# Optimization experiments

Measured on AMD Instinct MI355X. Metric: run time of the kernel, lower is better.

The kernel has to match this reference:

```python
import jax, jax.numpy as jnp
import numpy as np

B, N, C, S = 16, 1024, 16, 8
TYPE_DIM, TOK_DIM, D, O = 128, 128, 256, 256
NUM_TYPES, NUM_TOKENS, L = 200, 50000, 2
NEG = -1000000000000.0


def setup_inputs() -> dict:
    key = jax.random.key(0)
    ks = jax.random.split(key, 8)
    node_type = jax.random.randint(ks[0], (B, N), 0, NUM_TYPES)
    node_tokens = jax.random.randint(ks[1], (B, N, S), 0, NUM_TOKENS)
    children_index = jax.random.randint(ks[2], (B, N, C), 0, N)
    # padding_idx=0 -> row 0 of both embedding tables is zero
    type_table = (0.02 * jax.random.normal(ks[3], (NUM_TYPES, TYPE_DIM))).at[0].set(0.0)
    token_table = (0.02 * jax.random.normal(ks[4], (NUM_TOKENS, TOK_DIM))).at[0].set(0.0)
    W_parent = 0.02 * jax.random.normal(ks[5], (TYPE_DIM + TOK_DIM, D))
    b_parent = jnp.zeros((D,), jnp.float32)
    conv_w = 0.02 * jax.random.normal(ks[6], (L, 3, D, O))  # stacked [w_t, w_r, w_l] per layer
    conv_b = jnp.zeros((L, O), jnp.float32)
    attn_a = 0.02 * jax.random.normal(ks[7], (O,))
    return dict(node_type=node_type, node_tokens=node_tokens, children_index=children_index,
                type_table=type_table, token_table=token_table, W_parent=W_parent,
                b_parent=b_parent, conv_w=conv_w, conv_b=conv_b, attn_a=attn_a)


def _gather_children(parent, idx):
    # parent: [B,N,Dim]; idx: [B,N,C] with 0 meaning 'no child' (zero vector)
    lookup = parent.at[:, 0, :].set(0.0)
    return jax.vmap(lambda v, i: v[i])(lookup, idx)  # [B,N,C,Dim]


def _tbcnn_coef(children):
    # Standard TBCNN positional coefficients over [parent, child_1..child_C].
    b, n, c = children.shape
    f = jnp.float32
    cmask = (children > 0).astype(f)                                      # [B,N,C]
    mask = jnp.concatenate([jnp.zeros((b, n, 1), f), cmask], axis=2)      # [B,N,C+1]
    eta_t = jnp.concatenate([jnp.ones((b, n, 1), f), jnp.zeros((b, n, c), f)], axis=2)
    num_sib = jnp.sum(cmask, axis=2, keepdims=True)                       # [B,N,1]
    pos = jnp.arange(-1.0, c, dtype=f)                                    # [-1,0,...,C-1]
    child_idx = pos[None, None, :] * mask
    singles = jnp.concatenate([jnp.zeros((b, n, 1), f), jnp.full((b, n, 1), 0.5, f),
                               jnp.zeros((b, n, c - 1), f)], axis=2)
    denom = jnp.maximum(num_sib - 1.0, 1.0)
    eta_r = jnp.where(num_sib == 1.0, singles, mask * child_idx / denom)
    eta_l = (1.0 - eta_t) * (1.0 - eta_r) * mask
    return jnp.stack([eta_t, eta_r, eta_l], axis=3)                       # [B,N,C+1,3]


def _forward(node_type, node_tokens, children_index, type_table, token_table,
             W_parent, b_parent, conv_w, conv_b, attn_a):
    # --- embeddings + parent projection ---
    type_emb = type_table[node_type]                       # [B,N,TYPE_DIM]
    tok_emb = token_table[node_tokens].sum(axis=2)         # [B,N,TOK_DIM] (sum over subtokens)
    parent = jnp.concatenate([type_emb, tok_emb], axis=-1) @ W_parent + b_parent  # [B,N,D]
    # --- tree convolutions ---
    coef = _tbcnn_coef(children_index)                     # [B,N,C+1,3]
    nodes = parent
    ch = _gather_children(nodes, children_index)           # [B,N,C,D]
    n_layers = conv_w.shape[0]
    for l in range(n_layers):
        tree = jnp.concatenate([nodes[:, :, None, :], ch], axis=2)  # [B,N,C+1,D]
        mixed = jnp.einsum('bnck,bncd->bnkd', coef, tree)           # [B,N,3,D]
        nodes = jnp.tanh(jnp.einsum('bnkd,kdo->bno', mixed, conv_w[l]) + conv_b[l])
        if l < n_layers - 1:
            ch = _gather_children(nodes, children_index)
    # --- attention aggregation ---
    m = (node_type != 0)[..., None]                        # [B,N,1] bool
    score = jnp.einsum('bno,o->bn', nodes, attn_a)[..., None]
    score = jnp.where(m, score, NEG)
    w = jax.nn.sigmoid(score)
    code_vector = jnp.mean(nodes * m * w, axis=1)          # [B,O]
    return code_vector, nodes


def reference(node_type, node_tokens, children_index, type_table, token_table,
              W_parent, b_parent, conv_w, conv_b, attn_a):
    return _forward(node_type, node_tokens, children_index, type_table, token_table,
                    W_parent, b_parent, conv_w, conv_b, attn_a)
```

## Files before the change

### kernel.cpp

```cpp
#include <hip/hip_runtime.h>
#include <hip/hip_fp16.h>
#include <math.h>

constexpr int Bsz = 16, Nn = 1024, Cc = 16, Ss = 8;
constexpr int BN = Bsz * Nn;
constexpr int EQ = 32;
constexpr int CQ = 32;

typedef __attribute__((ext_vector_type(8))) short bf16x8;
typedef __attribute__((ext_vector_type(4))) float f32x4;
typedef __attribute__((ext_vector_type(4))) unsigned short u16x4;

__device__ inline unsigned short f2bf_rne(float x) {
    unsigned u = __builtin_bit_cast(unsigned, x);
    unsigned r = (u + 0x7FFFu + ((u >> 16) & 1u)) >> 16;
    return (unsigned short)r;
}
__device__ inline float bf2f(unsigned short h) {
    unsigned u = ((unsigned)h) << 16;
    return __builtin_bit_cast(float, u);
}

__global__ __launch_bounds__(256) void pack_all_kernel(
    const float* __restrict__ conv_w,
    const float* __restrict__ Wp,
    unsigned short* __restrict__ whi, unsigned short* __restrict__ wpq)
{
    if (blockIdx.x < 192) {
        const int t = blockIdx.x * 256 + threadIdx.x;
        const int col = t & 255;
        const int gg  = (t >> 8) & 3;
        const int kb  = (t >> 10) % 24;
        const int l   = t / (24 * 4 * 256);
        const float* W = conv_w + (size_t)l * 768 * 256;
        const size_t dst = (size_t)t * 8;
        #pragma unroll
        for (int i = 0; i < 8; ++i)
            whi[dst + i] = f2bf_rne(W[(size_t)(kb * 32 + gg * 8 + i) * 256 + col]);
    } else {
        const int t = (blockIdx.x - 192) * 256 + threadIdx.x;
        const int col = t & 255;
        const int gg  = (t >> 8) & 3;
        const int kb  = t >> 10;
        const size_t dst = (size_t)t * 8;
        #pragma unroll
        for (int i = 0; i < 8; ++i)
            wpq[dst + i] = f2bf_rne(Wp[(size_t)(kb * 32 + gg * 8 + i) * 256 + col]);
    }
}

__global__ __launch_bounds__(256, 4) void emb_mfma_kernel(
    const int* __restrict__ node_type, const int* __restrict__ node_tokens,
    const float* __restrict__ type_table, const float* __restrict__ token_table,
    const unsigned short* __restrict__ wpq,
    const float* __restrict__ bp,
    unsigned short* __restrict__ outh)
{
    constexpr int AP = 264;
    __shared__ unsigned short A[EQ][AP];

    const int tid  = threadIdx.x;
    const int lane = tid & 63;
    const int w    = tid >> 6;
    const int g0   = blockIdx.x * EQ;

    #pragma unroll
    for (int it = 0; it < 8; ++it) {
        const int r = w * 8 + it;
        const int gnode = g0 + r;
        if (lane < 32) {
            const int tt = node_type[gnode];
            const float4 v = *reinterpret_cast<const float4*>(
                type_table + (size_t)tt * 128 + lane * 4);
            u16x4 s;
            s.x = f2bf_rne(v.x); s.y = f2bf_rne(v.y);
            s.z = f2bf_rne(v.z); s.w = f2bf_rne(v.w);
            *reinterpret_cast<u16x4*>(&A[r][lane * 4]) = s;
        } else {
            const int q = lane - 32;
            float4 acc = {0.f, 0.f, 0.f, 0.f};
            #pragma unroll
            for (int si = 0; si < Ss; ++si) {
                const int tok = node_tokens[gnode * Ss + si];
                const float4 v = *reinterpret_cast<const float4*>(
                    token_table + (size_t)tok * 128 + q * 4);
                acc.x += v.x; acc.y += v.y; acc.z += v.z; acc.w += v.w;
            }
            u16x4 s;
            s.x = f2bf_rne(acc.x); s.y = f2bf_rne(acc.y);
            s.z = f2bf_rne(acc.z); s.w = f2bf_rne(acc.w);
            *reinterpret_cast<u16x4*>(&A[r][128 + q * 4]) = s;
        }
    }
    __syncthreads();

    const int colg = w * 64;
    const int rr   = lane & 15;
    const int g    = lane >> 4;

    const unsigned short* pwh = wpq + ((size_t)(g * 256 + colg + rr)) * 8;

    f32x4 acc[2][4];
    #pragma unroll
    for (int t = 0; t < 2; ++t)
        #pragma unroll
        for (int f = 0; f < 4; ++f) acc[t][f] = (f32x4){0.f, 0.f, 0.f, 0.f};

    bf16x8 bA[4], bB[4];
    #pragma unroll
    for (int f = 0; f < 4; ++f)
        bA[f] = *reinterpret_cast<const bf16x8*>(pwh + f * 128);

    for (int kb = 0; kb < 8; kb += 2) {
        {
            const int o1 = (kb + 1) * 8192;
            #pragma unroll
            for (int f = 0; f < 4; ++f)
                bB[f] = *reinterpret_cast<const bf16x8*>(pwh + o1 + f * 128);
        }
        {
            const int k0 = kb * 32 + g * 8;
            const bf16x8 a0 = *reinterpret_cast<const bf16x8*>(&A[rr][k0]);
            const bf16x8 a1 = *reinterpret_cast<const bf16x8*>(&A[16 + rr][k0]);
            #pragma unroll
            for (int f = 0; f < 4; ++f) {
                acc[0][f] = __builtin_amdgcn_mfma_f32_16x16x32_bf16(a0, bA[f], acc[0][f], 0, 0, 0);
                acc[1][f] = __builtin_amdgcn_mfma_f32_16x16x32_bf16(a1, bA[f], acc[1][f], 0, 0, 0);
            }
        }
        if (kb + 2 < 8) {
            const int o2 = (kb + 2) * 8192;
            #pragma unroll
            for (int f = 0; f < 4; ++f)
                bA[f] = *reinterpret_cast<const bf16x8*>(pwh + o2 + f * 128);
        }
        {
            const int k0 = (kb + 1) * 32 + g * 8;
            const bf16x8 a0 = *reinterpret_cast<const bf16x8*>(&A[rr][k0]);
            const bf16x8 a1 = *reinterpret_cast<const bf16x8*>(&A[16 + rr][k0]);
            #pragma unroll
            for (int f = 0; f < 4; ++f) {
                acc[0][f] = __builtin_amdgcn_mfma_f32_16x16x32_bf16(a0, bB[f], acc[0][f], 0, 0, 0);
                acc[1][f] = __builtin_amdgcn_mfma_f32_16x16x32_bf16(a1, bB[f], acc[1][f], 0, 0, 0);
            }
        }
    }

    #pragma unroll
    for (int t = 0; t < 2; ++t)
        #pragma unroll
        for (int f = 0; f < 4; ++f) {
            const int col = colg + f * 16 + rr;
            const float bv = bp[col];
            #pragma unroll
            for (int i = 0; i < 4; ++i) {
                const int row = t * 16 + g * 4 + i;
                outh[(size_t)(g0 + row) * 256 + col] = f2bf_rne(acc[t][f][i] + bv);
            }
        }
}

template<int FUSE>
__global__ __launch_bounds__(512, 4) void conv_mfma_kernel(
    const unsigned short* __restrict__ in_h,
    const int* __restrict__ children_index,
    const unsigned short* __restrict__ whi,
    const float* __restrict__ bias,
    unsigned short* __restrict__ out_h,
    float* __restrict__ out_f,
    const int* __restrict__ node_type,
    const float* __restrict__ attn_a,
    float* __restrict__ partial)
{
    constexpr int AP = 776;
    __shared__ unsigned short Ahi[CQ][AP];
    __shared__ unsigned short idx_s[CQ][Cc];
    __shared__ __half eta_s[2][CQ][Cc];
    __shared__ float sc_lds[8][CQ];
    __shared__ float wm_lds[CQ];

    const int tid = threadIdx.x;

    const int P = blockIdx.x;
    const int xx = P & 7;
    const int rst = P >> 3;
    const int j = rst & 31;
    const int yy = rst >> 5;
    const int batch = xx + 8 * yy;
    const int g0 = batch * Nn + j * CQ;
    const unsigned short* inb = in_h + (size_t)batch * Nn * 256;

    {
        const int r = tid >> 4, c = tid & 15;
        idx_s[r][c] = (unsigned short)children_index[(size_t)(g0 + r) * Cc + c];
    }
    __syncthreads();
    {
        const int r = tid >> 4, c = tid & 15;
        int ns = 0;
        #pragma unroll
        for (int q = 0; q < Cc; ++q) ns += (idx_s[r][q] > 0) ? 1 : 0;
        const bool cm = idx_s[r][c] > 0;
        float er;
        if (ns == 1) {
            er = (c == 0) ? 0.5f : 0.f;
        } else {
            const float denom = (float)((ns - 1 > 1) ? (ns - 1) : 1);
            er = (float)c / denom;
        }
        eta_s[0][r][c] = __float2half(cm ? er : 0.f);
        eta_s[1][r][c] = __float2half(cm ? (1.f - er) : 0.f);
    }
    __syncthreads();

    {
        const int q = tid & 63;
        const int rgrp = tid >> 6;
        #pragma unroll
        for (int rr4 = 0; rr4 < 4; ++rr4) {
            const int r = rgrp * 4 + rr4;
            const u16x4 m0h = *reinterpret_cast<const u16x4*>(
                in_h + (size_t)(g0 + r) * 256 + q * 4);
            float4 m1 = {0.f, 0.f, 0.f, 0.f};
            float4 m2 = {0.f, 0.f, 0.f, 0.f};
            #pragma unroll
            for (int c = 0; c < Cc; ++c) {
                const int ci = idx_s[r][c];
                const u16x4 vh = *reinterpret_cast<const u16x4*>(
                    inb + (size_t)ci * 256 + q * 4);
                const float vx = bf2f(vh.x), vy = bf2f(vh.y);
                const float vz = bf2f(vh.z), vw = bf2f(vh.w);
                const float er = __half2float(eta_s[0][r][c]);
                const float el = __half2float(eta_s[1][r][c]);
                m1.x = fmaf(er, vx, m1.x); m1.y = fmaf(er, vy, m1.y);
                m1.z = fmaf(er, vz, m1.z); m1.w = fmaf(er, vw, m1.w);
                m2.x = fmaf(el, vx, m2.x); m2.y = fmaf(el, vy, m2.y);
                m2.z = fmaf(el, vz, m2.z); m2.w = fmaf(el, vw, m2.w);
            }
            u16x4 s1, s2;
            s1.x = f2bf_rne(m1.x); s1.y = f2bf_rne(m1.y);
            s1.z = f2bf_rne(m1.z); s1.w = f2bf_rne(m1.w);
            s2.x = f2bf_rne(m2.x); s2.y = f2bf_rne(m2.y);
            s2.z = f2bf_rne(m2.z); s2.w = f2bf_rne(m2.w);
            *reinterpret_cast<u16x4*>(&Ahi[r][q * 4])       = m0h;
            *reinterpret_cast<u16x4*>(&Ahi[r][256 + q * 4]) = s1;
            *reinterpret_cast<u16x4*>(&Ahi[r][512 + q * 4]) = s2;
        }
    }
    __syncthreads();

    const int lane = tid & 63;
    const int w    = tid >> 6;
    const int colg = w * 32;
    const int rr   = lane & 15;
    const int g    = lane >> 4;

    const unsigned short* pwh = whi + ((size_t)(g * 256 + colg + rr)) * 8;

    f32x4 acc[2][2];
    #pragma unroll
    for (int t = 0; t < 2; ++t)
        #pragma unroll
        for (int f = 0; f < 2; ++f) acc[t][f] = (f32x4){0.f, 0.f, 0.f, 0.f};

    bf16x8 bA[2], bB[2];
    #pragma unroll
    for (int f = 0; f < 2; ++f)
        bA[f] = *reinterpret_cast<const bf16x8*>(pwh + f * 128);

    for (int kb = 0; kb < 24; kb += 2) {
        {
            const int o1 = (kb + 1) * 8192;
            #pragma unroll
            for (int f = 0; f < 2; ++f)
                bB[f] = *reinterpret_cast<const bf16x8*>(pwh + o1 + f * 128);
        }
        {
            const int k0 = kb * 32 + g * 8;
            const bf16x8 a0 = *reinterpret_cast<const bf16x8*>(&Ahi[rr][k0]);
            const bf16x8 a1 = *reinterpret_cast<const bf16x8*>(&Ahi[16 + rr][k0]);
            #pragma unroll
            for (int f = 0; f < 2; ++f) {
                acc[0][f] = __builtin_amdgcn_mfma_f32_16x16x32_bf16(a0, bA[f], acc[0][f], 0, 0, 0);
                acc[1][f] = __builtin_amdgcn_mfma_f32_16x16x32_bf16(a1, bA[f], acc[1][f], 0, 0, 0);
            }
        }
        if (kb + 2 < 24) {
            const int o2 = (kb + 2) * 8192;
            #pragma unroll
            for (int f = 0; f < 2; ++f)
                bA[f] = *reinterpret_cast<const bf16x8*>(pwh + o2 + f * 128);
        }
        {
            const int k0 = (kb + 1) * 32 + g * 8;
            const bf16x8 a0 = *reinterpret_cast<const bf16x8*>(&Ahi[rr][k0]);
            const bf16x8 a1 = *reinterpret_cast<const bf16x8*>(&Ahi[16 + rr][k0]);
            #pragma unroll
            for (int f = 0; f < 2; ++f) {
                acc[0][f] = __builtin_amdgcn_mfma_f32_16x16x32_bf16(a0, bB[f], acc[0][f], 0, 0, 0);
                acc[1][f] = __builtin_amdgcn_mfma_f32_16x16x32_bf16(a1, bB[f], acc[1][f], 0, 0, 0);
            }
        }
    }

    float nd[2][2][4];
    #pragma unroll
    for (int t = 0; t < 2; ++t)
        #pragma unroll
        for (int f = 0; f < 2; ++f) {
            const int col = colg + f * 16 + rr;
            const float bv = bias[col];
            #pragma unroll
            for (int i = 0; i < 4; ++i) {
                const int row = t * 16 + g * 4 + i;
                const float v = tanhf(acc[t][f][i] + bv);
                nd[t][f][i] = v;
                if (FUSE) out_f[(size_t)(g0 + row) * 256 + col] = v;
                else      out_h[(size_t)(g0 + row) * 256 + col] = f2bf_rne(v);
            }
        }

    if (FUSE) {
        float av[2];
        #pragma unroll
        for (int f = 0; f < 2; ++f) av[f] = attn_a[colg + f * 16 + rr];

        float s[2][4];
        #pragma unroll
        for (int t = 0; t < 2; ++t)
            #pragma unroll
            for (int i = 0; i < 4; ++i) {
                float v = 0.f;
                #pragma unroll
                for (int f = 0; f < 2; ++f) v = fmaf(nd[t][f][i], av[f], v);
                s[t][i] = v;
            }
        #pragma unroll
        for (int off = 1; off < 16; off <<= 1)
            #pragma unroll
            for (int t = 0; t < 2; ++t)
                #pragma unroll
                for (int i = 0; i < 4; ++i)
                    s[t][i] += __shfl_xor(s[t][i], off, 64);
        if (rr == 0) {
            #pragma unroll
            for (int t = 0; t < 2; ++t)
                #pragma unroll
                for (int i = 0; i < 4; ++i)
                    sc_lds[w][t * 16 + g * 4 + i] = s[t][i];
        }
        __syncthreads();
        if (tid < CQ) {
            float sc = 0.f;
            #pragma unroll
            for (int ww = 0; ww < 8; ++ww) sc += sc_lds[ww][tid];
            float wmv = 0.f;
            if (node_type[g0 + tid] != 0) wmv = 1.f / (1.f + expf(-sc));
            wm_lds[tid] = wmv;
        }
        __syncthreads();

        float qf[2];
        #pragma unroll
        for (int f = 0; f < 2; ++f) {
            float v = 0.f;
            #pragma unroll
            for (int t = 0; t < 2; ++t)
                #pragma unroll
                for (int i = 0; i < 4; ++i)
                    v = fmaf(wm_lds[t * 16 + g * 4 + i], nd[t][f][i], v);
            qf[f] = v;
        }
        #pragma unroll
        for (int f = 0; f < 2; ++f) {
            qf[f] += __shfl_xor(qf[f], 16, 64);
            qf[f] += __shfl_xor(qf[f], 32, 64);
        }
        if (g == 0) {
            const int pidx = batch * 32 + j;
            #pragma unroll
            for (int f = 0; f < 2; ++f)
                partial[(size_t)pidx * 256 + colg + f * 16 + rr] = qf[f];
        }
    }
}

__global__ __launch_bounds__(256) void final_kernel(
    const float* __restrict__ partial, float* __restrict__ code)
{
    const int i = blockIdx.x * 256 + threadIdx.x;
    const int b = i >> 8, o = i & 255;
    float acc = 0.f;
    #pragma unroll
    for (int c = 0; c < 32; ++c) acc += partial[(size_t)(b * 32 + c) * 256 + o];
    code[i] = acc * (1.f / 1024.f);
}

extern "C" void kernel_launch(void* const* d_in, const int* in_sizes, int n_in,
                              void* d_out, int out_size, void* d_ws, size_t ws_size,
                              hipStream_t stream)
{
    const int*   node_type   = (const int*)d_in[0];
    const int*   node_tokens = (const int*)d_in[1];
    const int*   children    = (const int*)d_in[2];
    const float* type_table  = (const float*)d_in[3];
    const float* token_table = (const float*)d_in[4];
    const float* Wp          = (const float*)d_in[5];
    const float* bp          = (const float*)d_in[6];
    const float* conv_w      = (const float*)d_in[7];
    const float* conv_b      = (const float*)d_in[8];
    const float* attn_a      = (const float*)d_in[9];

    float* out    = (float*)d_out;
    float* code   = out;
    float* nodesF = out + 4096;

    unsigned short* nodes0 = (unsigned short*)d_ws;
    unsigned short* nodes1 = nodes0 + (size_t)BN * 256;
    float* partial = (float*)(nodes1 + (size_t)BN * 256);
    unsigned short* whi = (unsigned short*)(partial + 512 * 256);
    unsigned short* wpq = whi + 2 * 196608;

    constexpr int LSTRIDE = 196608;

    pack_all_kernel<<<224, 256, 0, stream>>>(conv_w, Wp, whi, wpq);

    emb_mfma_kernel<<<BN / EQ, 256, 0, stream>>>(
        node_type, node_tokens, type_table, token_table, wpq, bp, nodes0);

    conv_mfma_kernel<0><<<BN / CQ, 512, 0, stream>>>(
        nodes0, children, whi, conv_b, nodes1,
        nullptr, nullptr, nullptr, nullptr);

    conv_mfma_kernel<1><<<BN / CQ, 512, 0, stream>>>(
        nodes1, children, whi + LSTRIDE, conv_b + 256, nullptr,
        nodesF, node_type, attn_a, partial);

    final_kernel<<<16, 256, 0, stream>>>(partial, code);
}
```

Baseline: 77.58 us.

## Halve embedding tile rows, use fast tanh/sigmoid, fp32 eta, MFMA priority

```diff
diff --git a/kernel.cpp b/kernel.cpp
--- a/kernel.cpp
+++ b/kernel.cpp
@@ -1,10 +1,9 @@
 #include <hip/hip_runtime.h>
-#include <hip/hip_fp16.h>
 #include <math.h>
 
 constexpr int Bsz = 16, Nn = 1024, Cc = 16, Ss = 8;
 constexpr int BN = Bsz * Nn;
-constexpr int EQ = 32;
+constexpr int EQ = 16;
 constexpr int CQ = 32;
 
 typedef __attribute__((ext_vector_type(8))) short bf16x8;
@@ -19,6 +18,12 @@
 __device__ inline float bf2f(unsigned short h) {
     unsigned u = ((unsigned)h) << 16;
     return __builtin_bit_cast(float, u);
+}
+__device__ inline float fast_tanh(float x) {
+    const float ax = fabsf(x);
+    const float t  = __expf(-2.f * ax);
+    const float r  = __fdividef(1.f - t, 1.f + t);
+    return copysignf(r, x);
 }
 
 __global__ __launch_bounds__(256) void pack_all_kernel(
@@ -65,8 +70,8 @@
     const int g0   = blockIdx.x * EQ;
 
     #pragma unroll
-    for (int it = 0; it < 8; ++it) {
-        const int r = w * 8 + it;
+    for (int it = 0; it < 4; ++it) {
+        const int r = w * 4 + it;
         const int gnode = g0 + r;
         if (lane < 32) {
             const int tt = node_type[gnode];
@@ -100,11 +105,9 @@
 
     const unsigned short* pwh = wpq + ((size_t)(g * 256 + colg + rr)) * 8;
 
-    f32x4 acc[2][4];
-    #pragma unroll
-    for (int t = 0; t < 2; ++t)
-        #pragma unroll
-        for (int f = 0; f < 4; ++f) acc[t][f] = (f32x4){0.f, 0.f, 0.f, 0.f};
+    f32x4 acc[4];
+    #pragma unroll
+    for (int f = 0; f < 4; ++f) acc[f] = (f32x4){0.f, 0.f, 0.f, 0.f};
 
     bf16x8 bA[4], bB[4];
     #pragma unroll
@@ -120,13 +123,10 @@
         }
         {
             const int k0 = kb * 32 + g * 8;
-            const bf16x8 a0 = *reinterpret_cast<const bf16x8*>(&A[rr][k0]);
-            const bf16x8 a1 = *reinterpret_cast<const bf16x8*>(&A[16 + rr][k0]);
-            #pragma unroll
-            for (int f = 0; f < 4; ++f) {
-                acc[0][f] = __builtin_amdgcn_mfma_f32_16x16x32_bf16(a0, bA[f], acc[0][f], 0, 0, 0);
-                acc[1][f] = __builtin_amdgcn_mfma_f32_16x16x32_bf16(a1, bA[f], acc[1][f], 0, 0, 0);
-            }
+            const bf16x8 ah = *reinterpret_cast<const bf16x8*>(&A[rr][k0]);
+            #pragma unroll
+            for (int f = 0; f < 4; ++f)
+                acc[f] = __builtin_amdgcn_mfma_f32_16x16x32_bf16(ah, bA[f], acc[f], 0, 0, 0);
         }
         if (kb + 2 < 8) {
             const int o2 = (kb + 2) * 8192;
@@ -136,28 +136,23 @@
         }
         {
             const int k0 = (kb + 1) * 32 + g * 8;
-            const bf16x8 a0 = *reinterpret_cast<const bf16x8*>(&A[rr][k0]);
-            const bf16x8 a1 = *reinterpret_cast<const bf16x8*>(&A[16 + rr][k0]);
-            #pragma unroll
-            for (int f = 0; f < 4; ++f) {
-                acc[0][f] = __builtin_amdgcn_mfma_f32_16x16x32_bf16(a0, bB[f], acc[0][f], 0, 0, 0);
-                acc[1][f] = __builtin_amdgcn_mfma_f32_16x16x32_bf16(a1, bB[f], acc[1][f], 0, 0, 0);
-            }
-        }
-    }
-
-    #pragma unroll
-    for (int t = 0; t < 2; ++t)
-        #pragma unroll
-        for (int f = 0; f < 4; ++f) {
-            const int col = colg + f * 16 + rr;
-            const float bv = bp[col];
-            #pragma unroll
-            for (int i = 0; i < 4; ++i) {
-                const int row = t * 16 + g * 4 + i;
-                outh[(size_t)(g0 + row) * 256 + col] = f2bf_rne(acc[t][f][i] + bv);
-            }
-        }
+            const bf16x8 ah = *reinterpret_cast<const bf16x8*>(&A[rr][k0]);
+            #pragma unroll
+            for (int f = 0; f < 4; ++f)
+                acc[f] = __builtin_amdgcn_mfma_f32_16x16x32_bf16(ah, bB[f], acc[f], 0, 0, 0);
+        }
+    }
+
+    #pragma unroll
+    for (int f = 0; f < 4; ++f) {
+        const int col = colg + f * 16 + rr;
+        const float bv = bp[col];
+        #pragma unroll
+        for (int i = 0; i < 4; ++i) {
+            const int row = g * 4 + i;
+            outh[(size_t)(g0 + row) * 256 + col] = f2bf_rne(acc[f][i] + bv);
+        }
+    }
 }
 
 template<int FUSE>
@@ -175,7 +170,8 @@
     constexpr int AP = 776;
     __shared__ unsigned short Ahi[CQ][AP];
     __shared__ unsigned short idx_s[CQ][Cc];
-    __shared__ __half eta_s[2][CQ][Cc];
+    __shared__ float etar_s[CQ][Cc];
+    __shared__ float etal_s[CQ][Cc];
     __shared__ float sc_lds[8][CQ];
     __shared__ float wm_lds[CQ];
 
@@ -208,8 +204,8 @@
             const float denom = (float)((ns - 1 > 1) ? (ns - 1) : 1);
             er = (float)c / denom;
         }
-        eta_s[0][r][c] = __float2half(cm ? er : 0.f);
-        eta_s[1][r][c] = __float2half(cm ? (1.f - er) : 0.f);
+        etar_s[r][c] = cm ? er : 0.f;
+        etal_s[r][c] = cm ? (1.f - er) : 0.f;
     }
     __syncthreads();
 
@@ -230,8 +226,8 @@
                     inb + (size_t)ci * 256 + q * 4);
                 const float vx = bf2f(vh.x), vy = bf2f(vh.y);
                 const float vz = bf2f(vh.z), vw = bf2f(vh.w);
-                const float er = __half2float(eta_s[0][r][c]);
-                const float el = __half2float(eta_s[1][r][c]);
+                const float er = etar_s[r][c];
+                const float el = etal_s[r][c];
                 m1.x = fmaf(er, vx, m1.x); m1.y = fmaf(er, vy, m1.y);
                 m1.z = fmaf(er, vz, m1.z); m1.w = fmaf(er, vw, m1.w);
                 m2.x = fmaf(el, vx, m2.x); m2.y = fmaf(el, vy, m2.y);
@@ -268,6 +264,7 @@
     for (int f = 0; f < 2; ++f)
         bA[f] = *reinterpret_cast<const bf16x8*>(pwh + f * 128);
 
+    __builtin_amdgcn_s_setprio(1);
     for (int kb = 0; kb < 24; kb += 2) {
         {
             const int o1 = (kb + 1) * 8192;
@@ -302,6 +299,7 @@
             }
         }
     }
+    __builtin_amdgcn_s_setprio(0);
 
     float nd[2][2][4];
     #pragma unroll
@@ -313,7 +311,7 @@
             #pragma unroll
             for (int i = 0; i < 4; ++i) {
                 const int row = t * 16 + g * 4 + i;
-                const float v = tanhf(acc[t][f][i] + bv);
+                const float v = fast_tanh(acc[t][f][i] + bv);
                 nd[t][f][i] = v;
                 if (FUSE) out_f[(size_t)(g0 + row) * 256 + col] = v;
                 else      out_h[(size_t)(g0 + row) * 256 + col] = f2bf_rne(v);
@@ -355,7 +353,8 @@
             #pragma unroll
             for (int ww = 0; ww < 8; ++ww) sc += sc_lds[ww][tid];
             float wmv = 0.f;
-            if (node_type[g0 + tid] != 0) wmv = 1.f / (1.f + expf(-sc));
+            if (node_type[g0 + tid] != 0)
+                wmv = __fdividef(1.f, 1.f + __expf(-sc));
             wm_lds[tid] = wmv;
         }
         __syncthreads();
```

After: 70.73 us. 8.8% less time.
